# Kernel tuning notes

Measured on AMD Instinct MI355X. Metric: run time of the kernel, lower is better.

## Reference

```python
import jax, jax.numpy as jnp
import numpy as np

HEADS = 16
D_MODEL = 1024
D_K = D_MODEL // HEADS


def setup_inputs() -> dict:
    key = jax.random.key(0)
    ks = jax.random.split(key, 8)
    B, S = 4, 2048
    scale = 1.0 / np.sqrt(D_MODEL)
    return {
        "queries": jax.random.normal(ks[0], (B, S, D_MODEL), dtype=jnp.float32),
        "keys": jax.random.normal(ks[1], (B, S, D_MODEL), dtype=jnp.float32),
        "values": jax.random.normal(ks[2], (B, S, D_MODEL), dtype=jnp.float32),
        # Per-head projection weights, stacked over heads: [H, d_model, d_k]
        "Wq": jax.random.normal(ks[3], (HEADS, D_MODEL, D_K), dtype=jnp.float32) * scale,
        "Wk": jax.random.normal(ks[4], (HEADS, D_MODEL, D_K), dtype=jnp.float32) * scale,
        "Wv": jax.random.normal(ks[5], (HEADS, D_MODEL, D_K), dtype=jnp.float32) * scale,
        "Wout": jax.random.normal(ks[6], (D_MODEL, D_MODEL), dtype=jnp.float32) * scale,
        "bout": jax.random.normal(ks[7], (D_MODEL,), dtype=jnp.float32) * 0.01,
    }


def reference(queries, keys, values, Wq, Wk, Wv, Wout, bout):
    # Per-head linear projections (torch Linear: x @ W.T, here W stored as [H, d_model, d_k])
    q = jnp.einsum("bsd,hdk->bhsk", queries, Wq)   # [B,H,S,d_k]
    k = jnp.einsum("btd,hdk->bhtk", keys, Wk)      # [B,H,T,d_k]
    v = jnp.einsum("btd,hdv->bhtv", values, Wv)    # [B,H,T,d_v]
    scores = jnp.einsum("bhsk,bhtk->bhst", q, k) / jnp.sqrt(jnp.float32(D_K))
    probs = jax.nn.softmax(scores, axis=-1)        # [B,H,S,T]
    wv = jnp.einsum("bhst,bhtv->bhsv", probs, v)   # [B,H,S,d_v]
    # concat heads along last dim: [B,S,H*d_v] == [B,S,d_model]
    B, H, S, Dv = wv.shape
    concat = jnp.transpose(wv, (0, 2, 1, 3)).reshape(B, S, H * Dv)
    return concat @ Wout.T + bout
```

## Files before the change

### kernel.cpp

```cpp
#include <hip/hip_runtime.h>
#include <hip/hip_bf16.h>
#include <stdint.h>

#define DM 1024
#define SZ ((size_t)8192*1024)
#define WSZ ((size_t)1024*1024)

typedef float  f32x4  __attribute__((ext_vector_type(4)));
typedef float  f32x16 __attribute__((ext_vector_type(16)));
typedef __bf16 bf16x8 __attribute__((ext_vector_type(8)));
typedef __bf16 bf16x2 __attribute__((ext_vector_type(2)));
typedef short  s16x8  __attribute__((ext_vector_type(8)));
typedef unsigned int u32;
typedef unsigned int u32x4 __attribute__((ext_vector_type(4)));

typedef const __attribute__((address_space(1))) void* gas_ptr;
typedef __attribute__((address_space(3))) void* las_ptr;

static __device__ __forceinline__ f32x4 mfma16(s16x8 a, s16x8 b, f32x4 c){
  return __builtin_amdgcn_mfma_f32_16x16x32_bf16(
      __builtin_bit_cast(bf16x8, a), __builtin_bit_cast(bf16x8, b), c, 0, 0, 0);
}
static __device__ __forceinline__ f32x16 mfma32(s16x8 a, s16x8 b, f32x16 c){
  return __builtin_amdgcn_mfma_f32_32x32x16_bf16(
      __builtin_bit_cast(bf16x8, a), __builtin_bit_cast(bf16x8, b), c, 0, 0, 0);
}

static __device__ __forceinline__ u32 pack2(float a, float b){
  bf16x2 v = { (__bf16)a, (__bf16)b };
  return __builtin_bit_cast(u32, v);
}
static __device__ __forceinline__ short f2bf(float f){
  __bf16 v = (__bf16)f;
  return __builtin_bit_cast(short, v);
}

static __device__ __forceinline__ void gload_lds16(void* l, const void* g){
  __builtin_amdgcn_global_load_lds((gas_ptr)g, (las_ptr)l, 16, 0, 0);
}

#define QSCALE 0.1803368801111444f


__global__ void convert_misc(const float* __restrict__ q, const float* __restrict__ k,
                             const float* __restrict__ v, const float* __restrict__ wo,
                             short* __restrict__ ws){
  size_t c = (size_t)blockIdx.x*blockDim.x + threadIdx.x;
  const size_t n8_in = 3*(SZ/8);
  const float* src; short* dst;
  if (c < n8_in){
    int s = (int)(c >> 20);
    size_t off = c*8 - ((size_t)s << 23);
    src = (s==0 ? q : (s==1 ? k : v)) + off;
    dst = ws + c*8;
  } else {
    size_t off = (c - n8_in)*8;
    src = wo + off;
    dst = ws + 6*SZ + 3*WSZ + off;
  }
  float4 a = *(const float4*)src;
  float4 b = *(const float4*)(src + 4);
  uint4 o;
  o.x = pack2(a.x, a.y); o.y = pack2(a.z, a.w);
  o.z = pack2(b.x, b.y); o.w = pack2(b.z, b.w);
  *(uint4*)dst = o;
}

__global__ void convert_wqkv(const float* __restrict__ wq, const float* __restrict__ wk,
                             const float* __restrict__ wv, short* __restrict__ ws){
  __shared__ float tile[64][65];
  int bid = blockIdx.x;
  int sel = bid >> 8;
  int h   = (bid >> 4) & 15;
  int dt  = bid & 15;
  const float* W = sel==0 ? wq : (sel==1 ? wk : wv);
  float sc = sel==0 ? QSCALE : 1.0f;
  short* Bt = ws + 6*SZ + (size_t)sel*WSZ;
  int tid = threadIdx.x;
  int r = tid >> 4, c4 = (tid & 15)*4;
  int d0 = dt*64;
  #pragma unroll
  for (int i=0;i<4;i++){
    int d = r + i*16;
    float4 vv = *(const float4*)&W[(size_t)h*65536 + (size_t)(d0+d)*64 + c4];
    tile[d][c4+0]=vv.x*sc; tile[d][c4+1]=vv.y*sc; tile[d][c4+2]=vv.z*sc; tile[d][c4+3]=vv.w*sc;
  }
  __syncthreads();
  #pragma unroll
  for (int i=0;i<4;i++){
    int kk = r + i*16;
    unsigned int lo = pack2(tile[c4+0][kk], tile[c4+1][kk]);
    unsigned int hi = pack2(tile[c4+2][kk], tile[c4+3][kk]);
    *(uint2*)&Bt[(size_t)(h*64+kk)*1024 + d0 + c4] = make_uint2(lo, hi);
  }
}


static __device__ __forceinline__ void gemm_core_bf16(
    const short* __restrict__ A, const short* __restrict__ Bt,
    int bm, int bn, short* As, short* Bs, f32x4 acc[4][4])
{
  int tid = threadIdx.x;
  int w = tid>>6, lane = tid&63;
  int wm = w>>1, wn = w&1;
  int col = lane&15, kg = lane>>4;
  int rs = w*16 + (lane>>2);
  int ch = lane&3;
  int chs = ch ^ (rs & 3);

  auto stage = [&](int buf, int kt){
    #pragma unroll
    for (int it=0; it<2; ++it){
      int r = rs + it*64;
      gload_lds16(As + buf*4096 + r*32 + ch*8,
                  A + (size_t)(bm*128 + r)*1024 + kt*32 + chs*8);
    }
    #pragma unroll
    for (int it=0; it<2; ++it){
      int r = rs + it*64;
      gload_lds16(Bs + buf*4096 + r*32 + ch*8,
                  Bt + (size_t)(bn*128 + r)*1024 + kt*32 + chs*8);
    }
  };

  const f32x4 fzero = {0.f,0.f,0.f,0.f};
  #pragma unroll
  for (int mf=0; mf<4; ++mf)
    #pragma unroll
    for (int nf=0; nf<4; ++nf)
      acc[mf][nf] = fzero;

  int fbase = col*32 + ((kg ^ (col&3))<<3);

  stage(0, 0);
  int buf = 0;
  for (int kt=0; kt<32; ++kt){
    __syncthreads();
    if (kt < 31) stage(buf^1, kt+1);
    s16x8 af[4], bfr[4];
    #pragma unroll
    for (int mf=0; mf<4; ++mf)
      af[mf] = *(const s16x8*)(As + buf*4096 + (wm*64 + mf*16)*32 + fbase);
    #pragma unroll
    for (int nf=0; nf<4; ++nf)
      bfr[nf] = *(const s16x8*)(Bs + buf*4096 + (wn*64 + nf*16)*32 + fbase);
    #pragma unroll
    for (int mf=0; mf<4; ++mf)
      #pragma unroll
      for (int nf=0; nf<4; ++nf)
        acc[mf][nf] = mfma16(af[mf], bfr[nf], acc[mf][nf]);
    buf ^= 1;
  }
}

__global__ __launch_bounds__(256,2) void gemm_qkv(short* __restrict__ ws){
  __shared__ __align__(16) short As[2*4096];
  __shared__ __align__(16) short Bs[2*4096];
  int bid = blockIdx.x;
  bid = (bid & 7)*192 + (bid >> 3);
  int bm = bid / 24, bnq = bid % 24;
  int sel = bnq >> 3, bn = bnq & 7;
  const short* A  = ws + (size_t)sel*SZ;
  const short* Bt = ws + 6*SZ + (size_t)sel*WSZ;
  f32x4 acc[4][4];
  gemm_core_bf16(A, Bt, bm, bn, As, Bs, acc);

  int tid = threadIdx.x, w = tid>>6, lane = tid&63;
  int wm=w>>1, wn=w&1, col=lane&15, kg=lane>>4;
  if (sel == 0){
    short* O = ws + 3*SZ;
    #pragma unroll
    for (int mf=0; mf<4; ++mf){
      int gr0 = bm*128 + wm*64 + mf*16 + kg*4;
      #pragma unroll
      for (int nf=0; nf<4; ++nf){
        int gc = bn*128 + wn*64 + nf*16 + col;
        #pragma unroll
        for (int r=0; r<4; ++r)
          O[(size_t)(gr0+r)*1024 + gc] = f2bf(acc[mf][nf][r]);
      }
    }
  } else if (sel == 1){
    short* Kt = ws + 4*SZ;
    #pragma unroll
    for (int mf=0; mf<4; ++mf){
      int gr0 = bm*128 + wm*64 + mf*16 + kg*4;
      int b = gr0 >> 11, s0 = gr0 & 2047;
      int ts = s0 >> 5, t0 = s0 & 31;
      #pragma unroll
      for (int nf=0; nf<4; ++nf){
        int gc = bn*128 + wn*64 + nf*16 + col;
        int h = gc >> 6, d = gc & 63;
        size_t base = ((size_t)((b*16+h)*64 + ts))*2048 + (size_t)((d>>3)*32)*8 + (d&7);
        #pragma unroll
        for (int r=0; r<4; ++r)
          Kt[base + (size_t)(t0+r)*8] = f2bf(acc[mf][nf][r]);
      }
    }
  } else {
    short* Vt = ws + 5*SZ;
    #pragma unroll
    for (int mf=0; mf<4; ++mf){
      int gr0 = bm*128 + wm*64 + mf*16 + kg*4;
      int b = gr0 >> 11, s0 = gr0 & 2047;
      int ts = s0 >> 5, c2 = (s0 >> 3) & 3, j0 = s0 & 7;
      #pragma unroll
      for (int nf=0; nf<4; ++nf){
        int gc = bn*128 + wn*64 + nf*16 + col;
        int h = gc >> 6, dv = gc & 63;
        unsigned int lo = pack2(acc[mf][nf][0], acc[mf][nf][1]);
        unsigned int hi = pack2(acc[mf][nf][2], acc[mf][nf][3]);
        size_t addr = ((size_t)((b*16+h)*64 + ts))*2048 + (size_t)(c2*64 + dv)*8 + j0;
        *(uint2*)&Vt[addr] = make_uint2(lo, hi);
      }
    }
  }
}

__global__ __launch_bounds__(256,2) void gemm_out(const short* __restrict__ cc,
                                                  const short* __restrict__ BtO,
                                                  const float* __restrict__ bias,
                                                  float* __restrict__ out){
  __shared__ __align__(16) short As[2*4096];
  __shared__ __align__(16) short Bs[2*4096];
  int bid = blockIdx.x;
  bid = (bid & 7)*64 + (bid >> 3);
  int bm = bid >> 3, bn = bid & 7;
  f32x4 acc[4][4];
  gemm_core_bf16(cc, BtO, bm, bn, As, Bs, acc);

  int tid = threadIdx.x, w=tid>>6, lane=tid&63;
  int wm=w>>1, wn=w&1, col=lane&15, kg=lane>>4;
  #pragma unroll
  for (int nf=0; nf<4; ++nf){
    int gc = bn*128 + wn*64 + nf*16 + col;
    float bb = bias[gc];
    #pragma unroll
    for (int mf=0; mf<4; ++mf){
      int gr0 = bm*128 + wm*64 + mf*16 + kg*4;
      #pragma unroll
      for (int r=0; r<4; ++r)
        out[(size_t)(gr0+r)*1024 + gc] = acc[mf][nf][r] + bb;
    }
  }
}

__global__ __launch_bounds__(256,4) void attn(const short* __restrict__ qp,
                                              const short* __restrict__ kpT,
                                              const short* __restrict__ vTt,
                                              short* __restrict__ cc){
  __shared__ __align__(16) short Ks[2][2048];
  __shared__ __align__(16) short Vs[2][2048];
  int bid = blockIdx.x;
  bid = (bid & 7)*128 + (bid >> 3);
  int qb = bid & 15, h = (bid>>4) & 15, b = bid >> 8;
  int bh = b*16 + h;
  int tid = threadIdx.x, w = tid>>6, lane = tid&63;
  int ql = lane & 31, hi = lane >> 5;
  int qbase = qb*128 + w*32;

  const short* qg = qp + ((size_t)(b*2048 + qbase + ql))*1024 + h*64;
  s16x8 qf[4];
  #pragma unroll
  for (int ks=0; ks<4; ++ks)
    qf[ks] = *(const s16x8*)(qg + ks*16 + hi*8);

  const short* ktb = kpT + ((size_t)(bh*64))*2048;
  const short* vtb = vTt + ((size_t)(bh*64))*2048;

  int koff = hi*512 + ql*16;
  int voff = hi*1024 + ql*16;

  int jj = (w & 1) * 1024;
  const short* ksrcb = ktb + jj + lane*8;
  const short* vsrcb = vtb + jj + lane*8;
  auto stageK = [&](int buf, int ti){
    if (w < 2){
      const short* src = ksrcb + (size_t)ti*2048;
      short* dst = &Ks[buf][jj + lane*8];
      gload_lds16(dst, src);
      gload_lds16(dst + 512, src + 512);
    }
  };
  auto stageV = [&](int buf, int ti){
    if (w >= 2){
      const short* src = vsrcb + (size_t)ti*2048;
      short* dst = &Vs[buf][jj + lane*8];
      gload_lds16(dst, src);
      gload_lds16(dst + 512, src + 512);
    }
  };

  const f32x16 z16 = {0.f,0.f,0.f,0.f,0.f,0.f,0.f,0.f,
                      0.f,0.f,0.f,0.f,0.f,0.f,0.f,0.f};
  f32x16 o0 = z16, o1 = z16;
  float l = 0.f;
  f32x16 sA, sB;

  auto packP = [&](f32x16& s, s16x8* pb){
    u32 a0 = pack2(s[0], s[1]),  b0 = pack2(s[2], s[3]);
    u32 c0 = pack2(s[4], s[5]),  d0 = pack2(s[6], s[7]);
    asm("v_permlane32_swap_b32 %0, %1" : "+v"(a0), "+v"(c0));
    asm("v_permlane32_swap_b32 %0, %1" : "+v"(b0), "+v"(d0));
    u32x4 t0v = {a0, b0, c0, d0};
    pb[0] = __builtin_bit_cast(s16x8, t0v);
    u32 a1 = pack2(s[8], s[9]),   b1 = pack2(s[10], s[11]);
    u32 c1 = pack2(s[12], s[13]), d1 = pack2(s[14], s[15]);
    asm("v_permlane32_swap_b32 %0, %1" : "+v"(a1), "+v"(c1));
    asm("v_permlane32_swap_b32 %0, %1" : "+v"(b1), "+v"(d1));
    u32x4 t1v = {a1, b1, c1, d1};
    pb[1] = __builtin_bit_cast(s16x8, t1v);
  };

  auto iter = [&](int t, int bufV, int bufKn, f32x16& si, f32x16& so){
    __syncthreads();
    if (t+2 < 64) stageK(bufV, t+2);
    if (t+1 < 64) stageV(bufKn, t+1);

    float la=0.f, lb=0.f, lc=0.f, ld=0.f;
    #pragma unroll
    for (int i=0;i<16;i+=4){
      si[i]   = __builtin_amdgcn_exp2f(si[i]);   la += si[i];
      si[i+1] = __builtin_amdgcn_exp2f(si[i+1]); lb += si[i+1];
      si[i+2] = __builtin_amdgcn_exp2f(si[i+2]); lc += si[i+2];
      si[i+3] = __builtin_amdgcn_exp2f(si[i+3]); ld += si[i+3];
    }
    l += (la+lb)+(lc+ld);

    s16x8 pb[2];
    packP(si, pb);

    const char* kt = (const char*)(&Ks[bufKn][0]);
    const char* vt = (const char*)(&Vs[bufV][0]);
    __builtin_amdgcn_s_setprio(1);
    so = z16;
    if (t+1 < 64){
      #pragma unroll
      for (int ks=0; ks<4; ++ks){
        s16x8 kf = *(const s16x8*)(kt + koff + ks*1024);
        so = mfma32(kf, qf[ks], so);
      }
    }
    #pragma unroll
    for (int ks2=0; ks2<2; ++ks2){
      s16x8 vf0 = *(const s16x8*)(vt + voff + ks2*2048);
      s16x8 vf1 = *(const s16x8*)(vt + voff + ks2*2048 + 512);
      o0 = mfma32(vf0, pb[ks2], o0);
      o1 = mfma32(vf1, pb[ks2], o1);
    }
    __builtin_amdgcn_s_setprio(0);
  };

  stageK(0, 0);
  stageV(0, 0);
  stageK(1, 1);
  __syncthreads();
  {
    const char* kt = (const char*)(&Ks[0][0]);
    sA = z16;
    #pragma unroll
    for (int ks=0; ks<4; ++ks){
      s16x8 kf = *(const s16x8*)(kt + koff + ks*1024);
      sA = mfma32(kf, qf[ks], sA);
    }
  }
  for (int t = 0; t < 64; t += 2){
    iter(t,   0, 1, sA, sB);
    iter(t+1, 1, 0, sB, sA);
  }

  l += __shfl_xor(l, 32);
  float rcl = 1.0f / l;
  short* og = cc + ((size_t)(b*2048 + qbase + ql))*1024 + h*64;
  #pragma unroll
  for (int s=0; s<4; ++s){
    int dv0 = s*8 + hi*4;
    uint2 w0, w1;
    w0.x = pack2(o0[s*4+0]*rcl, o0[s*4+1]*rcl);
    w0.y = pack2(o0[s*4+2]*rcl, o0[s*4+3]*rcl);
    *(uint2*)&og[dv0] = w0;
    w1.x = pack2(o1[s*4+0]*rcl, o1[s*4+1]*rcl);
    w1.y = pack2(o1[s*4+2]*rcl, o1[s*4+3]*rcl);
    *(uint2*)&og[32 + dv0] = w1;
  }
}


extern "C" void kernel_launch(void* const* d_in, const int* in_sizes, int n_in,
                              void* d_out, int out_size, void* d_ws, size_t ws_size,
                              hipStream_t stream){
  const float* q  = (const float*)d_in[0];
  const float* k  = (const float*)d_in[1];
  const float* v  = (const float*)d_in[2];
  const float* wq = (const float*)d_in[3];
  const float* wk = (const float*)d_in[4];
  const float* wv = (const float*)d_in[5];
  const float* wo = (const float*)d_in[6];
  const float* bo = (const float*)d_in[7];
  short* ws = (short*)d_ws;
  float* out = (float*)d_out;

  size_t needed = (6*SZ + 4*WSZ)*sizeof(short);
  if (ws_size < needed) return;

  convert_misc<<<12800, 256, 0, stream>>>(q, k, v, wo, ws);
  convert_wqkv<<<768, 256, 0, stream>>>(wq, wk, wv, ws);
  gemm_qkv<<<1536, 256, 0, stream>>>(ws);
  attn<<<1024, 256, 0, stream>>>(ws + 3*SZ, ws + 4*SZ, ws + 5*SZ, ws);
  gemm_out<<<512, 256, 0, stream>>>(ws, ws + 6*SZ + 3*WSZ, bo, out);
}
```

Baseline: 204.8 us.

## Double KV tile size and restructure attention loop into a simple double-buffered body

The attention kernel now processes 64-key tiles (two 32-key sub-tiles) per iteration instead of 32, which halves the number of barriers and the loop iterations. It replaces the software-pipelined QK/PV overlap (computing the next tile's scores during the current PV) with a straightforward stage-next-then-compute body, and all four waves now issue loads for K or V. Row-sum accumulation uses packed float2 adds. Launch bounds drop occupancy from 4 to 2 blocks per CU and LDS per block doubles, which gives up latency hiding from occupancy and the previous cross-tile MFMA/exp overlap.

```diff
diff --git a/kernel.cpp b/kernel.cpp
--- a/kernel.cpp
+++ b/kernel.cpp
@@ -6,6 +6,7 @@
 #define SZ ((size_t)8192*1024)
 #define WSZ ((size_t)1024*1024)
 
+typedef float  f32x2  __attribute__((ext_vector_type(2)));
 typedef float  f32x4  __attribute__((ext_vector_type(4)));
 typedef float  f32x16 __attribute__((ext_vector_type(16)));
 typedef __bf16 bf16x8 __attribute__((ext_vector_type(8)));
@@ -245,12 +246,12 @@
   }
 }
 
-__global__ __launch_bounds__(256,4) void attn(const short* __restrict__ qp,
+__global__ __launch_bounds__(256,2) void attn(const short* __restrict__ qp,
                                               const short* __restrict__ kpT,
                                               const short* __restrict__ vTt,
                                               short* __restrict__ cc){
-  __shared__ __align__(16) short Ks[2][2048];
-  __shared__ __align__(16) short Vs[2][2048];
+  __shared__ __align__(16) short Ks[2][4096];
+  __shared__ __align__(16) short Vs[2][4096];
   int bid = blockIdx.x;
   bid = (bid & 7)*128 + (bid >> 3);
   int qb = bid & 15, h = (bid>>4) & 15, b = bid >> 8;
@@ -271,31 +272,22 @@
   int koff = hi*512 + ql*16;
   int voff = hi*1024 + ql*16;
 
-  int jj = (w & 1) * 1024;
-  const short* ksrcb = ktb + jj + lane*8;
-  const short* vsrcb = vtb + jj + lane*8;
-  auto stageK = [&](int buf, int ti){
-    if (w < 2){
-      const short* src = ksrcb + (size_t)ti*2048;
-      short* dst = &Ks[buf][jj + lane*8];
-      gload_lds16(dst, src);
-      gload_lds16(dst + 512, src + 512);
-    }
-  };
-  auto stageV = [&](int buf, int ti){
-    if (w >= 2){
-      const short* src = vsrcb + (size_t)ti*2048;
-      short* dst = &Vs[buf][jj + lane*8];
-      gload_lds16(dst, src);
-      gload_lds16(dst + 512, src + 512);
-    }
+  int jj = (w & 1) * 2048;
+  const short* sgb = ((w < 2) ? ktb : vtb) + jj + lane*8;
+  short* ldb = ((w < 2) ? &Ks[0][0] : &Vs[0][0]) + jj + lane*8;
+  auto stage = [&](int buf, int ti2){
+    const short* src = sgb + (size_t)ti2*4096;
+    short* dst = ldb + buf*4096;
+    gload_lds16(dst,        src);
+    gload_lds16(dst + 512,  src + 512);
+    gload_lds16(dst + 1024, src + 1024);
+    gload_lds16(dst + 1536, src + 1536);
   };
 
   const f32x16 z16 = {0.f,0.f,0.f,0.f,0.f,0.f,0.f,0.f,
                       0.f,0.f,0.f,0.f,0.f,0.f,0.f,0.f};
   f32x16 o0 = z16, o1 = z16;
-  float l = 0.f;
-  f32x16 sA, sB;
+  f32x2 l2 = {0.f, 0.f};
 
   auto packP = [&](f32x16& s, s16x8* pb){
     u32 a0 = pack2(s[0], s[1]),  b0 = pack2(s[2], s[3]);
@@ -312,63 +304,65 @@
     pb[1] = __builtin_bit_cast(s16x8, t1v);
   };
 
-  auto iter = [&](int t, int bufV, int bufKn, f32x16& si, f32x16& so){
-    __syncthreads();
-    if (t+2 < 64) stageK(bufV, t+2);
-    if (t+1 < 64) stageV(bufKn, t+1);
-
-    float la=0.f, lb=0.f, lc=0.f, ld=0.f;
+  auto body = [&](int buf){
+    const char* kt = (const char*)Ks + buf*8192;
+    const char* vt = (const char*)Vs + buf*8192;
+    f32x16 s0 = z16, s1 = z16;
+    __builtin_amdgcn_s_setprio(1);
+    #pragma unroll
+    for (int ks=0; ks<4; ++ks){
+      s16x8 kf0 = *(const s16x8*)(kt + koff + ks*1024);
+      s16x8 kf1 = *(const s16x8*)(kt + 4096 + koff + ks*1024);
+      s0 = mfma32(kf0, qf[ks], s0);
+      s1 = mfma32(kf1, qf[ks], s1);
+    }
+    __builtin_amdgcn_s_setprio(0);
+
+    f32x2 la = {0.f,0.f}, lb = {0.f,0.f};
     #pragma unroll
     for (int i=0;i<16;i+=4){
-      si[i]   = __builtin_amdgcn_exp2f(si[i]);   la += si[i];
-      si[i+1] = __builtin_amdgcn_exp2f(si[i+1]); lb += si[i+1];
-      si[i+2] = __builtin_amdgcn_exp2f(si[i+2]); lc += si[i+2];
-      si[i+3] = __builtin_amdgcn_exp2f(si[i+3]); ld += si[i+3];
-    }
-    l += (la+lb)+(lc+ld);
-
-    s16x8 pb[2];
-    packP(si, pb);
-
-    const char* kt = (const char*)(&Ks[bufKn][0]);
-    const char* vt = (const char*)(&Vs[bufV][0]);
+      s0[i]   = __builtin_amdgcn_exp2f(s0[i]);
+      s0[i+1] = __builtin_amdgcn_exp2f(s0[i+1]);
+      s0[i+2] = __builtin_amdgcn_exp2f(s0[i+2]);
+      s0[i+3] = __builtin_amdgcn_exp2f(s0[i+3]);
+      f32x2 pa = {s0[i], s0[i+1]}, pbv = {s0[i+2], s0[i+3]};
+      la += pa; lb += pbv;
+    }
+    #pragma unroll
+    for (int i=0;i<16;i+=4){
+      s1[i]   = __builtin_amdgcn_exp2f(s1[i]);
+      s1[i+1] = __builtin_amdgcn_exp2f(s1[i+1]);
+      s1[i+2] = __builtin_amdgcn_exp2f(s1[i+2]);
+      s1[i+3] = __builtin_amdgcn_exp2f(s1[i+3]);
+      f32x2 pa = {s1[i], s1[i+1]}, pbv = {s1[i+2], s1[i+3]};
+      la += pa; lb += pbv;
+    }
+    l2 += la + lb;
+
+    s16x8 pb[4];
+    packP(s0, pb);
+    packP(s1, pb + 2);
+
     __builtin_amdgcn_s_setprio(1);
-    so = z16;
-    if (t+1 < 64){
-      #pragma unroll
-      for (int ks=0; ks<4; ++ks){
-        s16x8 kf = *(const s16x8*)(kt + koff + ks*1024);
-        so = mfma32(kf, qf[ks], so);
-      }
-    }
-    #pragma unroll
-    for (int ks2=0; ks2<2; ++ks2){
-      s16x8 vf0 = *(const s16x8*)(vt + voff + ks2*2048);
-      s16x8 vf1 = *(const s16x8*)(vt + voff + ks2*2048 + 512);
+    #pragma unroll
+    for (int ks2=0; ks2<4; ++ks2){
+      const char* vb2 = vt + (ks2>>1)*4096 + (ks2&1)*2048 + voff;
+      s16x8 vf0 = *(const s16x8*)(vb2);
+      s16x8 vf1 = *(const s16x8*)(vb2 + 512);
       o0 = mfma32(vf0, pb[ks2], o0);
       o1 = mfma32(vf1, pb[ks2], o1);
     }
     __builtin_amdgcn_s_setprio(0);
   };
 
-  stageK(0, 0);
-  stageV(0, 0);
-  stageK(1, 1);
-  __syncthreads();
-  {
-    const char* kt = (const char*)(&Ks[0][0]);
-    sA = z16;
-    #pragma unroll
-    for (int ks=0; ks<4; ++ks){
-      s16x8 kf = *(const s16x8*)(kt + koff + ks*1024);
-      sA = mfma32(kf, qf[ks], sA);
-    }
-  }
-  for (int t = 0; t < 64; t += 2){
-    iter(t,   0, 1, sA, sB);
-    iter(t+1, 1, 0, sB, sA);
-  }
-
+  stage(0, 0);
+  for (int ti = 0; ti < 32; ++ti){
+    __syncthreads();
+    if (ti < 31) stage((ti&1)^1, ti+1);
+    body(ti&1);
+  }
+
+  float l = l2[0] + l2[1];
   l += __shfl_xor(l, 32);
   float rcl = 1.0f / l;
   short* og = cc + ((size_t)(b*2048 + qbase + ql))*1024 + h*64;
```

Result: no change. 203.3 us (-0.7%).
